# Performance work log

Measured on AMD Instinct MI355X. Metric: run time of the kernel, lower is better.

The kernel has to match this reference:

```python
import jax, jax.numpy as jnp
import numpy as np

N_NODES = 20000
N_EDGES = 400000
B = 4            # number of edge_attr tensors in the Python loop (batch of graphs)
NODE_DIM = 256   # == hidden_dim (required: forward feeds raw x into edge_fc)
EDGE_DIM = 16
HIDDEN = 256
OUT_DIM = 128


def setup_inputs() -> dict:
    key = jax.random.key(0)
    ks = jax.random.split(key, 6)
    x = jax.random.normal(ks[0], (N_NODES, NODE_DIM), dtype=jnp.float32)
    edge_index = jax.random.randint(ks[1], (2, N_EDGES), 0, N_NODES, dtype=jnp.int64)
    edge_attrs = jax.random.normal(ks[2], (B, N_EDGES, EDGE_DIM), dtype=jnp.float32)
    fan_in = 2 * HIDDEN + EDGE_DIM  # edge_fc in_features
    W_edge = jax.random.normal(ks[3], (fan_in, HIDDEN), dtype=jnp.float32) / np.sqrt(fan_in).astype(np.float32)
    b_edge = jnp.zeros((HIDDEN,), dtype=jnp.float32)
    W_graph = jax.random.normal(ks[4], (HIDDEN, OUT_DIM), dtype=jnp.float32) / np.sqrt(HIDDEN).astype(np.float32)
    b_graph = jnp.zeros((OUT_DIM,), dtype=jnp.float32)
    return {"x": x, "edge_index": edge_index, "edge_attrs": edge_attrs,
            "W_edge": W_edge, "b_edge": b_edge, "W_graph": W_graph, "b_graph": b_graph}


def reference(x, edge_index, edge_attrs, W_edge, b_edge, W_graph, b_graph):
    # Original: for each edge_attr in edge_attrs:
    #   relu(cat([x[src], x[dst], edge_attr]) @ W_edge + b).mean(0) @ W_graph + b_graph
    # Equivalent: split W_edge by the concat blocks; the (src,dst) contribution is
    # shared across the batch, so compute it once and broadcast.
    D = x.shape[1]
    W_src, W_dst, W_attr = W_edge[:D], W_edge[D:2 * D], W_edge[2 * D:]
    src = x[edge_index[0]]                      # [E, D] gather
    dst = x[edge_index[1]]                      # [E, D] gather
    base = src @ W_src + dst @ W_dst + b_edge   # [E, H]
    h = jax.nn.relu(base[None, :, :] + jnp.einsum('bea,ah->beh', edge_attrs, W_attr))  # [B, E, H]
    graph_feat = h.mean(axis=1)                 # [B, H] mean pool over edges
    return graph_feat @ W_graph + b_graph       # [B, OUT]
```

## Files before the change

### kernel.cpp

```cpp
#include <hip/hip_runtime.h>
#include <hip/hip_bf16.h>

#define N_NODES 20000
#define N_EDGES 400000
#define NODE_DIM 256
#define HIDDEN 256
#define OUT_DIM 128
#define PROJ_BLOCKS 628

typedef __attribute__((ext_vector_type(8))) short short8;
typedef __attribute__((ext_vector_type(4))) float f32x4;

__device__ inline unsigned f2bf_pk(float a, float b) {
  __hip_bfloat162 h = __float22bfloat162_rn(float2{a, b});
  union { __hip_bfloat162 h; unsigned u; } v;
  v.h = h;
  return v.u;
}
__device__ inline unsigned short f2bf(float f) {
  union { float f; unsigned u; } v; v.f = f;
  unsigned r = (v.u + 0x7FFFu + ((v.u >> 16) & 1u)) >> 16;
  return (unsigned short)r;
}

__global__ __launch_bounds__(256) void proj_mfma(
    const float* __restrict__ x, const float* __restrict__ We,
    const float* __restrict__ be, unsigned short* __restrict__ C,
    float* __restrict__ partial) {
  const int tid = threadIdx.x;
  if (blockIdx.x == 0) {
    for (int i = tid; i < 4 * HIDDEN; i += 256) partial[i] = 0.f;
  }
  const int bm = blockIdx.x >> 2;
  const int bn = blockIdx.x & 3;
  const int row0 = bm * 128;
  const int col0 = bn * 128;
  const int half = col0 >> 8;
  const int ncol0 = col0 & 255;
  const int lane = tid & 63, wave = tid >> 6;
  const int q = lane >> 4, c = lane & 15;
  const int wm = wave >> 1, wn = wave & 1;

  __shared__ unsigned short As[128][40];
  __shared__ unsigned short Bs[128][40];

  f32x4 acc[4][4];
#pragma unroll
  for (int i = 0; i < 4; ++i)
#pragma unroll
    for (int t = 0; t < 4; ++t) acc[i][t] = (f32x4){0.f, 0.f, 0.f, 0.f};

  const int ar = tid >> 1;
  const int ak = (tid & 1) * 16;
  const int bk = tid >> 3;
  const int bn0 = (tid & 7) * 16;

  for (int k0 = 0; k0 < NODE_DIM; k0 += 32) {
    {
      const int r = row0 + ar;
      union { short8 s; unsigned u[4]; } t0, t1;
      if (r < N_NODES) {
        const float4* src = (const float4*)&x[(size_t)r * NODE_DIM + k0 + ak];
        float4 f0 = src[0], f1 = src[1], f2 = src[2], f3 = src[3];
        t0.u[0] = f2bf_pk(f0.x, f0.y); t0.u[1] = f2bf_pk(f0.z, f0.w);
        t0.u[2] = f2bf_pk(f1.x, f1.y); t0.u[3] = f2bf_pk(f1.z, f1.w);
        t1.u[0] = f2bf_pk(f2.x, f2.y); t1.u[1] = f2bf_pk(f2.z, f2.w);
        t1.u[2] = f2bf_pk(f3.x, f3.y); t1.u[3] = f2bf_pk(f3.z, f3.w);
      } else {
        t0.u[0] = t0.u[1] = t0.u[2] = t0.u[3] = 0u;
        t1.u[0] = t1.u[1] = t1.u[2] = t1.u[3] = 0u;
      }
      *(short8*)&As[ar][ak] = t0.s;
      *(short8*)&As[ar][ak + 8] = t1.s;
    }
    {
      const float4* src = (const float4*)&We[(size_t)(half * 256 + k0 + bk) * HIDDEN + ncol0 + bn0];
#pragma unroll
      for (int v = 0; v < 4; ++v) {
        float4 f = src[v];
        Bs[bn0 + v * 4 + 0][bk] = f2bf(f.x);
        Bs[bn0 + v * 4 + 1][bk] = f2bf(f.y);
        Bs[bn0 + v * 4 + 2][bk] = f2bf(f.z);
        Bs[bn0 + v * 4 + 3][bk] = f2bf(f.w);
      }
    }
    __syncthreads();
    short8 Af[4], Bf[4];
#pragma unroll
    for (int i = 0; i < 4; ++i) Af[i] = *(const short8*)&As[wm * 64 + i * 16 + c][q * 8];
#pragma unroll
    for (int t = 0; t < 4; ++t) Bf[t] = *(const short8*)&Bs[wn * 64 + t * 16 + c][q * 8];
#pragma unroll
    for (int i = 0; i < 4; ++i)
#pragma unroll
      for (int t = 0; t < 4; ++t)
        acc[i][t] = __builtin_amdgcn_mfma_f32_16x16x32_bf16(Af[i], Bf[t], acc[i][t], 0, 0, 0);
    __syncthreads();
  }

  float biasv[4] = {0.f, 0.f, 0.f, 0.f};
  const int nbase = ncol0 + wn * 64;
  if (half) {
#pragma unroll
    for (int t = 0; t < 4; ++t) biasv[t] = be[nbase + t * 16 + c];
  }
#pragma unroll
  for (int i = 0; i < 4; ++i) {
#pragma unroll
    for (int r = 0; r < 4; ++r) {
      const int node = row0 + wm * 64 + i * 16 + q * 4 + r;
      if (node < N_NODES) {
        union { ushort4 o; unsigned u[2]; } w;
        w.u[0] = f2bf_pk(acc[i][0][r] + biasv[0], acc[i][1][r] + biasv[1]);
        w.u[1] = f2bf_pk(acc[i][2][r] + biasv[2], acc[i][3][r] + biasv[3]);
        *(ushort4*)&C[(size_t)node * 512 + half * 256 + nbase + c * 4] = w.o;
      }
    }
  }
}

__global__ __launch_bounds__(256) void edge_mfma(
    const unsigned short* __restrict__ C, const int* __restrict__ ei,
    const float* __restrict__ attrs, const float* __restrict__ We,
    float* __restrict__ partial) {
  const int tid = threadIdx.x;
  const int lane = tid & 63, wave = tid >> 6;
  const int q = lane >> 4, c = lane & 15;
  const int hb = wave * 64;

  short8 Bf[4];
#pragma unroll
  for (int t = 0; t < 4; ++t) {
    short8 bf;
#pragma unroll
    for (int j = 0; j < 8; ++j) {
      int k = q * 8 + j;
      float w = (k < 16) ? We[(size_t)(512 + k) * HIDDEN + hb + t * 16 + c] : 0.0f;
      bf[j] = (short)f2bf(w);
    }
    Bf[t] = bf;
  }

  f32x4 acc4[4][4];
#pragma unroll
  for (int b = 0; b < 4; ++b)
#pragma unroll
    for (int t = 0; t < 4; ++t) acc4[b][t] = (f32x4){0.f, 0.f, 0.f, 0.f};

  const f32x4 zero4 = {0.f, 0.f, 0.f, 0.f};
  const int ngroups = N_EDGES / 16;
  int g = blockIdx.x;
  int4 ns4 = make_int4(0, 0, 0, 0), nd4 = ns4;
  if (g < ngroups) {
    ns4 = *(const int4*)&ei[g * 16 + q * 4];
    nd4 = *(const int4*)&ei[N_EDGES + g * 16 + q * 4];
  }
  while (g < ngroups) {
    const int e0 = g * 16;
    const int gn = g + gridDim.x;
    int4 ns4n = ns4, nd4n = nd4;
    if (gn < ngroups) {
      ns4n = *(const int4*)&ei[gn * 16 + q * 4];
      nd4n = *(const int4*)&ei[N_EDGES + gn * 16 + q * 4];
    }

    f32x4 base4[4];
    {
      const int nn[4] = {ns4.x, ns4.y, ns4.z, ns4.w};
      const int dd[4] = {nd4.x, nd4.y, nd4.z, nd4.w};
#pragma unroll
      for (int r = 0; r < 4; ++r) {
        const uint2 s = *(const uint2*)&C[(size_t)nn[r] * 512 + hb + c * 4];
        const uint2 d = *(const uint2*)&C[(size_t)dd[r] * 512 + 256 + hb + c * 4];
        base4[0][r] = __uint_as_float(s.x << 16) + __uint_as_float(d.x << 16);
        base4[1][r] = __uint_as_float(s.x & 0xFFFF0000u) + __uint_as_float(d.x & 0xFFFF0000u);
        base4[2][r] = __uint_as_float(s.y << 16) + __uint_as_float(d.y << 16);
        base4[3][r] = __uint_as_float(s.y & 0xFFFF0000u) + __uint_as_float(d.y & 0xFFFF0000u);
      }
    }

    short8 Af[4];
    if (q < 2) {
#pragma unroll
      for (int b = 0; b < 4; ++b) {
        const size_t off = ((size_t)b * N_EDGES + e0 + c) * 16 + q * 8;
        const float4 a0 = *(const float4*)&attrs[off];
        const float4 a1 = *(const float4*)&attrs[off + 4];
        union { short8 s; unsigned u[4]; } af;
        af.u[0] = f2bf_pk(a0.x, a0.y); af.u[1] = f2bf_pk(a0.z, a0.w);
        af.u[2] = f2bf_pk(a1.x, a1.y); af.u[3] = f2bf_pk(a1.z, a1.w);
        Af[b] = af.s;
      }
    } else {
      short8 z;
#pragma unroll
      for (int j = 0; j < 8; ++j) z[j] = 0;
#pragma unroll
      for (int b = 0; b < 4; ++b) Af[b] = z;
    }

#pragma unroll
    for (int b = 0; b < 4; ++b) {
#pragma unroll
      for (int t = 0; t < 4; ++t) {
        f32x4 S = __builtin_amdgcn_mfma_f32_16x16x32_bf16(Af[b], Bf[t], zero4, 0, 0, 0);
        f32x4 u = S + base4[t];
        u[0] = fmaxf(u[0], 0.f); u[1] = fmaxf(u[1], 0.f);
        u[2] = fmaxf(u[2], 0.f); u[3] = fmaxf(u[3], 0.f);
        acc4[b][t] += u;
      }
    }
    ns4 = ns4n; nd4 = nd4n; g = gn;
  }

#pragma unroll
  for (int b = 0; b < 4; ++b)
#pragma unroll
    for (int t = 0; t < 4; ++t) {
      float v = acc4[b][t][0] + acc4[b][t][1] + acc4[b][t][2] + acc4[b][t][3];
      v += __shfl_xor(v, 16, 64);
      v += __shfl_xor(v, 32, 64);
      if (q == 0) atomicAdd(&partial[b * HIDDEN + hb + t * 16 + c], v);
    }
}

__global__ __launch_bounds__(256) void graph_out(
    const float* __restrict__ partial, const float* __restrict__ Wg,
    const float* __restrict__ bg, float* __restrict__ out) {
  const int o = blockIdx.x;
  const int hh = threadIdx.x;
  const int lane = hh & 63, wave = hh >> 6;
  const float w = Wg[(size_t)hh * OUT_DIM + o];
  float v[4];
#pragma unroll
  for (int b = 0; b < 4; ++b) v[b] = partial[b * HIDDEN + hh] * w;
#pragma unroll
  for (int off = 32; off >= 1; off >>= 1)
#pragma unroll
    for (int b = 0; b < 4; ++b) v[b] += __shfl_down(v[b], off, 64);
  __shared__ float red[4][4];
  if (lane == 0)
#pragma unroll
    for (int b = 0; b < 4; ++b) red[wave][b] = v[b];
  __syncthreads();
  if (hh < 4) {
    float s = red[0][hh] + red[1][hh] + red[2][hh] + red[3][hh];
    out[hh * OUT_DIM + o] = s * (1.0f / (float)N_EDGES) + bg[o];
  }
}

extern "C" void kernel_launch(void* const* d_in, const int* in_sizes, int n_in,
                              void* d_out, int out_size, void* d_ws, size_t ws_size,
                              hipStream_t stream) {
  const float* x  = (const float*)d_in[0];
  const int*   ei = (const int*)d_in[1];
  const float* ea = (const float*)d_in[2];
  const float* We = (const float*)d_in[3];
  const float* be = (const float*)d_in[4];
  const float* Wg = (const float*)d_in[5];
  const float* bg = (const float*)d_in[6];
  float* out = (float*)d_out;

  unsigned short* C = (unsigned short*)d_ws;
  float* partial = (float*)((char*)d_ws + (size_t)N_NODES * 512 * 2);

  proj_mfma<<<PROJ_BLOCKS, 256, 0, stream>>>(x, We, be, C, partial);
  edge_mfma<<<2500, 256, 0, stream>>>(C, ei, ea, We, partial);
  graph_out<<<128, 256, 0, stream>>>(partial, Wg, bg, out);
}
```

Baseline: 291.3 us.

## Pre-transpose W to bf16 and pre-convert edge attrs in a prep kernel

Adds a prep kernel that transposes and converts the node-projection weights to bf16 once, zeroes the partial sums, and, if the workspace is large enough, converts all edge attributes to bf16. proj_mfma now loads B tiles with vector bf16 loads instead of scalar conversions and transposed LDS stores. edge_mfma reads bf16 attrs when they are available and drops the software prefetch of edge indices. The attr conversion pass reads fp32 and writes bf16 before edge_mfma reads the bf16 copy back, so total traffic on that path rises.

```diff
diff --git a/kernel.cpp b/kernel.cpp
--- a/kernel.cpp
+++ b/kernel.cpp
@@ -6,7 +6,6 @@
 #define NODE_DIM 256
 #define HIDDEN 256
 #define OUT_DIM 128
-#define PROJ_BLOCKS 628
 
 typedef __attribute__((ext_vector_type(8))) short short8;
 typedef __attribute__((ext_vector_type(4))) float f32x4;
@@ -23,20 +22,43 @@
   return (unsigned short)r;
 }
 
+template <bool CONV_ATTRS>
+__global__ __launch_bounds__(256) void prep(
+    const float* __restrict__ attrs, unsigned short* __restrict__ attrs_bf,
+    const float* __restrict__ We, unsigned short* __restrict__ Wt,
+    float* __restrict__ partial) {
+  const int tid = blockIdx.x * 256 + threadIdx.x;
+  if (blockIdx.x == 0) {
+    for (int i = threadIdx.x; i < 4 * HIDDEN; i += 256) partial[i] = 0.f;
+  }
+  if (tid < 512 * 256) {
+    const int n = tid >> 8, k = tid & 255;
+    const float w = (n < 256) ? We[(size_t)k * 256 + n]
+                              : We[(size_t)(256 + k) * 256 + (n - 256)];
+    Wt[tid] = f2bf(w);
+  }
+  if (CONV_ATTRS) {
+    const int nt = gridDim.x * 256;
+    const int total4 = 4 * N_EDGES * 16 / 4;
+    for (int i = tid; i < total4; i += nt) {
+      float4 v = ((const float4*)attrs)[i];
+      union { ushort4 o; unsigned u[2]; } w;
+      w.u[0] = f2bf_pk(v.x, v.y);
+      w.u[1] = f2bf_pk(v.z, v.w);
+      ((ushort4*)attrs_bf)[i] = w.o;
+    }
+  }
+}
+
 __global__ __launch_bounds__(256) void proj_mfma(
-    const float* __restrict__ x, const float* __restrict__ We,
-    const float* __restrict__ be, unsigned short* __restrict__ C,
-    float* __restrict__ partial) {
+    const float* __restrict__ x, const unsigned short* __restrict__ Wt,
+    const float* __restrict__ be, unsigned short* __restrict__ C) {
   const int tid = threadIdx.x;
-  if (blockIdx.x == 0) {
-    for (int i = tid; i < 4 * HIDDEN; i += 256) partial[i] = 0.f;
-  }
   const int bm = blockIdx.x >> 2;
-  const int bn = blockIdx.x & 3;
+  const int bnb = blockIdx.x & 3;
   const int row0 = bm * 128;
-  const int col0 = bn * 128;
+  const int col0 = bnb * 128;
   const int half = col0 >> 8;
-  const int ncol0 = col0 & 255;
   const int lane = tid & 63, wave = tid >> 6;
   const int q = lane >> 4, c = lane & 15;
   const int wm = wave >> 1, wn = wave & 1;
@@ -50,17 +72,15 @@
 #pragma unroll
     for (int t = 0; t < 4; ++t) acc[i][t] = (f32x4){0.f, 0.f, 0.f, 0.f};
 
-  const int ar = tid >> 1;
-  const int ak = (tid & 1) * 16;
-  const int bk = tid >> 3;
-  const int bn0 = (tid & 7) * 16;
+  const int sr = tid >> 1;
+  const int sk = (tid & 1) * 16;
 
   for (int k0 = 0; k0 < NODE_DIM; k0 += 32) {
     {
-      const int r = row0 + ar;
+      const int r = row0 + sr;
       union { short8 s; unsigned u[4]; } t0, t1;
       if (r < N_NODES) {
-        const float4* src = (const float4*)&x[(size_t)r * NODE_DIM + k0 + ak];
+        const float4* src = (const float4*)&x[(size_t)r * NODE_DIM + k0 + sk];
         float4 f0 = src[0], f1 = src[1], f2 = src[2], f3 = src[3];
         t0.u[0] = f2bf_pk(f0.x, f0.y); t0.u[1] = f2bf_pk(f0.z, f0.w);
         t0.u[2] = f2bf_pk(f1.x, f1.y); t0.u[3] = f2bf_pk(f1.z, f1.w);
@@ -70,19 +90,13 @@
         t0.u[0] = t0.u[1] = t0.u[2] = t0.u[3] = 0u;
         t1.u[0] = t1.u[1] = t1.u[2] = t1.u[3] = 0u;
       }
-      *(short8*)&As[ar][ak] = t0.s;
-      *(short8*)&As[ar][ak + 8] = t1.s;
+      *(short8*)&As[sr][sk] = t0.s;
+      *(short8*)&As[sr][sk + 8] = t1.s;
     }
     {
-      const float4* src = (const float4*)&We[(size_t)(half * 256 + k0 + bk) * HIDDEN + ncol0 + bn0];
-#pragma unroll
-      for (int v = 0; v < 4; ++v) {
-        float4 f = src[v];
-        Bs[bn0 + v * 4 + 0][bk] = f2bf(f.x);
-        Bs[bn0 + v * 4 + 1][bk] = f2bf(f.y);
-        Bs[bn0 + v * 4 + 2][bk] = f2bf(f.z);
-        Bs[bn0 + v * 4 + 3][bk] = f2bf(f.w);
-      }
+      const unsigned short* src = &Wt[(size_t)(col0 + sr) * 256 + k0 + sk];
+      *(short8*)&Bs[sr][sk] = *(const short8*)src;
+      *(short8*)&Bs[sr][sk + 8] = *(const short8*)(src + 8);
     }
     __syncthreads();
     short8 Af[4], Bf[4];
@@ -99,7 +113,7 @@
   }
 
   float biasv[4] = {0.f, 0.f, 0.f, 0.f};
-  const int nbase = ncol0 + wn * 64;
+  const int nbase = (col0 & 255) + wn * 64;
   if (half) {
 #pragma unroll
     for (int t = 0; t < 4; ++t) biasv[t] = be[nbase + t * 16 + c];
@@ -119,10 +133,11 @@
   }
 }
 
+template <bool PRE>
 __global__ __launch_bounds__(256) void edge_mfma(
     const unsigned short* __restrict__ C, const int* __restrict__ ei,
-    const float* __restrict__ attrs, const float* __restrict__ We,
-    float* __restrict__ partial) {
+    const float* __restrict__ attrs_f, const unsigned short* __restrict__ attrs_b,
+    const float* __restrict__ We, float* __restrict__ partial) {
   const int tid = threadIdx.x;
   const int lane = tid & 63, wave = tid >> 6;
   const int q = lane >> 4, c = lane & 15;
@@ -149,19 +164,35 @@
 
   const f32x4 zero4 = {0.f, 0.f, 0.f, 0.f};
   const int ngroups = N_EDGES / 16;
-  int g = blockIdx.x;
-  int4 ns4 = make_int4(0, 0, 0, 0), nd4 = ns4;
-  if (g < ngroups) {
-    ns4 = *(const int4*)&ei[g * 16 + q * 4];
-    nd4 = *(const int4*)&ei[N_EDGES + g * 16 + q * 4];
-  }
-  while (g < ngroups) {
+  for (int g = blockIdx.x; g < ngroups; g += gridDim.x) {
     const int e0 = g * 16;
-    const int gn = g + gridDim.x;
-    int4 ns4n = ns4, nd4n = nd4;
-    if (gn < ngroups) {
-      ns4n = *(const int4*)&ei[gn * 16 + q * 4];
-      nd4n = *(const int4*)&ei[N_EDGES + gn * 16 + q * 4];
+    const int4 ns4 = *(const int4*)&ei[e0 + q * 4];
+    const int4 nd4 = *(const int4*)&ei[N_EDGES + e0 + q * 4];
+
+    short8 Af[4];
+    if (q < 2) {
+      if (PRE) {
+#pragma unroll
+        for (int b = 0; b < 4; ++b)
+          Af[b] = *(const short8*)&attrs_b[((size_t)b * N_EDGES + e0 + c) * 16 + q * 8];
+      } else {
+#pragma unroll
+        for (int b = 0; b < 4; ++b) {
+          const size_t off = ((size_t)b * N_EDGES + e0 + c) * 16 + q * 8;
+          const float4 a0 = *(const float4*)&attrs_f[off];
+          const float4 a1 = *(const float4*)&attrs_f[off + 4];
+          union { short8 s; unsigned u[4]; } af;
+          af.u[0] = f2bf_pk(a0.x, a0.y); af.u[1] = f2bf_pk(a0.z, a0.w);
+          af.u[2] = f2bf_pk(a1.x, a1.y); af.u[3] = f2bf_pk(a1.z, a1.w);
+          Af[b] = af.s;
+        }
+      }
+    } else {
+      short8 z;
+#pragma unroll
+      for (int j = 0; j < 8; ++j) z[j] = 0;
+#pragma unroll
+      for (int b = 0; b < 4; ++b) Af[b] = z;
     }
 
     f32x4 base4[4];
@@ -179,26 +210,6 @@
       }
     }
 
-    short8 Af[4];
-    if (q < 2) {
-#pragma unroll
-      for (int b = 0; b < 4; ++b) {
-        const size_t off = ((size_t)b * N_EDGES + e0 + c) * 16 + q * 8;
-        const float4 a0 = *(const float4*)&attrs[off];
-        const float4 a1 = *(const float4*)&attrs[off + 4];
-        union { short8 s; unsigned u[4]; } af;
-        af.u[0] = f2bf_pk(a0.x, a0.y); af.u[1] = f2bf_pk(a0.z, a0.w);
-        af.u[2] = f2bf_pk(a1.x, a1.y); af.u[3] = f2bf_pk(a1.z, a1.w);
-        Af[b] = af.s;
-      }
-    } else {
-      short8 z;
-#pragma unroll
-      for (int j = 0; j < 8; ++j) z[j] = 0;
-#pragma unroll
-      for (int b = 0; b < 4; ++b) Af[b] = z;
-    }
-
 #pragma unroll
     for (int b = 0; b < 4; ++b) {
 #pragma unroll
@@ -210,7 +221,6 @@
         acc4[b][t] += u;
       }
     }
-    ns4 = ns4n; nd4 = nd4n; g = gn;
   }
 
 #pragma unroll
@@ -261,10 +271,25 @@
   const float* bg = (const float*)d_in[6];
   float* out = (float*)d_out;
 
-  unsigned short* C = (unsigned short*)d_ws;
-  float* partial = (float*)((char*)d_ws + (size_t)N_NODES * 512 * 2);
-
-  proj_mfma<<<PROJ_BLOCKS, 256, 0, stream>>>(x, We, be, C, partial);
-  edge_mfma<<<2500, 256, 0, stream>>>(C, ei, ea, We, partial);
+  const size_t C_bytes  = (size_t)N_NODES * 512 * 2;
+  const size_t Wt_bytes = (size_t)512 * 256 * 2;
+  const size_t P_bytes  = 4 * HIDDEN * sizeof(float);
+  const size_t A_bytes  = (size_t)4 * N_EDGES * 16 * 2;
+  unsigned short* C  = (unsigned short*)d_ws;
+  unsigned short* Wt = (unsigned short*)((char*)d_ws + C_bytes);
+  float* partial     = (float*)((char*)d_ws + C_bytes + Wt_bytes);
+  const bool pre = ws_size >= C_bytes + Wt_bytes + P_bytes + A_bytes;
+  unsigned short* attrs_bf =
+      pre ? (unsigned short*)((char*)d_ws + C_bytes + Wt_bytes + P_bytes) : nullptr;
+
+  if (pre)
+    prep<true><<<1024, 256, 0, stream>>>(ea, attrs_bf, We, Wt, partial);
+  else
+    prep<false><<<512, 256, 0, stream>>>(ea, nullptr, We, Wt, partial);
+  proj_mfma<<<157 * 4, 256, 0, stream>>>(x, Wt, be, C);
+  if (pre)
+    edge_mfma<true><<<2500, 256, 0, stream>>>(C, ei, nullptr, attrs_bf, We, partial);
+  else
+    edge_mfma<false><<<2500, 256, 0, stream>>>(C, ei, ea, nullptr, We, partial);
   graph_out<<<128, 256, 0, stream>>>(partial, Wg, bg, out);
 }
```

New measurement: 290.6 us. Within noise of the previous version (-0.2%).
